# Performance work log

Hardware: AMD Instinct MI355X
Metric: run time of the kernel (lower is better)

## Reference

```python
import jax, jax.numpy as jnp
import numpy as np

EPS = 1e-12  # torch F.normalize eps


def setup_inputs() -> dict:
    key = jax.random.key(0)
    k1, k2, k3 = jax.random.split(key, 3)
    N, C, H, W = 64, 512, 30, 30
    K = 64
    x = jax.random.normal(k1, (N, C, H, W), dtype=jnp.float32)
    # 1x1 conv weight [K, C] (kernel spatial dims squeezed out)
    conv_w = jax.random.normal(k2, (K, C), dtype=jnp.float32) * 0.04
    centroids = jax.random.uniform(k3, (K, C), dtype=jnp.float32)
    return {"x": x, "conv_w": conv_w, "centroids": centroids}


def reference(x, conv_w, centroids):
    N, C, H, W = x.shape
    K = conv_w.shape[0]
    # descriptor-wise L2 normalize over channel dim (normalize_input=True)
    nrm = jnp.sqrt(jnp.sum(x * x, axis=1, keepdims=True))
    x = x / jnp.maximum(nrm, EPS)
    xf = x.reshape(N, C, H * W)                       # [N, C, P]
    # 1x1 conv == per-pixel matmul: [N, K, P]
    logits = jnp.einsum("kc,ncp->nkp", conv_w, xf)
    a = jax.nn.softmax(logits, axis=1)                # softmax over clusters
    # vlad[n,k,c] = sum_p a[n,k,p] * (xf[n,c,p] - centroids[k,c])
    #            = (a @ xf^T) - sum_p(a) * centroids   (GEMM decomposition)
    agg = jnp.einsum("nkp,ncp->nkc", a, xf)           # [N, K, C]
    vlad = agg - a.sum(axis=-1)[:, :, None] * centroids[None]
    return vlad
```

## Files before the change

kernel.cpp:

```cpp
#include <hip/hip_runtime.h>
#include <math.h>

#define N_DIM 64
#define C_DIM 512
#define K_DIM 64
#define P_DIM 900
#define P_PAD 928
#define PTILES 15

typedef __attribute__((ext_vector_type(8))) short short8;
typedef __attribute__((ext_vector_type(4))) float f32x4;
typedef __attribute__((ext_vector_type(4))) uint  u32x4;

#define A2_ELEMS   ((size_t)N_DIM * K_DIM * P_PAD)

__device__ inline ushort f2bf(float f) {
  uint u = __builtin_bit_cast(uint, f);
  u += 0x7FFFu + ((u >> 16) & 1u);
  return (ushort)(u >> 16);
}
__device__ inline uint pk2(float a, float b) {
  return (uint)f2bf(a) | ((uint)f2bf(b) << 16);
}

__global__ __launch_bounds__(256, 2) void netvlad_assign(
    const float* __restrict__ x, const float* __restrict__ w,
    ushort* __restrict__ a2, float* __restrict__ asum_part)
{
  const int n = blockIdx.y, bpt = blockIdx.x, p0 = bpt * 64;
  const int tid = threadIdx.x, wave = tid >> 6, lane = tid & 63;
  const int l15 = lane & 15, lhi = lane >> 4;

  __shared__ float wredm[4][4][16];
  __shared__ float wreds[4][4][16];

  short8 wfrag[16];
  const float* wrow = w + (size_t)(wave * 16 + l15) * C_DIM + lhi * 8;
#pragma unroll
  for (int ks = 0; ks < 16; ++ks) {
    f32x4 f0 = *(const f32x4*)(wrow + ks * 32);
    f32x4 f1 = *(const f32x4*)(wrow + ks * 32 + 4);
    u32x4 up;
    up[0] = pk2(f0[0], f0[1]); up[1] = pk2(f0[2], f0[3]);
    up[2] = pk2(f1[0], f1[1]); up[3] = pk2(f1[2], f1[3]);
    wfrag[ks] = __builtin_bit_cast(short8, up);
  }

  const float* xb = x + (size_t)n * C_DIM * P_DIM;
  int pb = p0 + 4 * l15;
  if (pb > P_DIM - 4) pb = P_DIM - 4;
  const float* xbase = xb + pb + (size_t)(lhi * 8) * P_DIM;

  f32x4 acc[4];
#pragma unroll
  for (int pt = 0; pt < 4; ++pt) acc[pt] = (f32x4){0.f, 0.f, 0.f, 0.f};
  float ssqp[4] = {0.f, 0.f, 0.f, 0.f};

#pragma unroll
  for (int ks = 0; ks < 16; ++ks) {
    const float* src = xbase + (size_t)(ks * 32) * P_DIM;
    f32x4 xv0 = *(const f32x4*)(src + 0 * P_DIM);
    f32x4 xv1 = *(const f32x4*)(src + 1 * P_DIM);
    f32x4 xv2 = *(const f32x4*)(src + 2 * P_DIM);
    f32x4 xv3 = *(const f32x4*)(src + 3 * P_DIM);
    f32x4 xv4 = *(const f32x4*)(src + 4 * P_DIM);
    f32x4 xv5 = *(const f32x4*)(src + 5 * P_DIM);
    f32x4 xv6 = *(const f32x4*)(src + 6 * P_DIM);
    f32x4 xv7 = *(const f32x4*)(src + 7 * P_DIM);
#pragma unroll
    for (int pt = 0; pt < 4; ++pt) {
      ssqp[pt] += xv0[pt] * xv0[pt] + xv1[pt] * xv1[pt]
                + xv2[pt] * xv2[pt] + xv3[pt] * xv3[pt]
                + xv4[pt] * xv4[pt] + xv5[pt] * xv5[pt]
                + xv6[pt] * xv6[pt] + xv7[pt] * xv7[pt];
      u32x4 up;
      up[0] = pk2(xv0[pt], xv1[pt]); up[1] = pk2(xv2[pt], xv3[pt]);
      up[2] = pk2(xv4[pt], xv5[pt]); up[3] = pk2(xv6[pt], xv7[pt]);
      short8 xf = __builtin_bit_cast(short8, up);
      acc[pt] = __builtin_amdgcn_mfma_f32_16x16x32_bf16(wfrag[ks], xf, acc[pt], 0, 0, 0);
    }
  }

  float linv[4];
#pragma unroll
  for (int pt = 0; pt < 4; ++pt) {
    float s = ssqp[pt];
    s += __shfl_xor(s, 16);
    s += __shfl_xor(s, 32);
    linv[pt] = 1.0f / fmaxf(sqrtf(s), 1e-12f);
  }

  float lg[4][4];
#pragma unroll
  for (int pt = 0; pt < 4; ++pt) {
    float m = -1e30f;
#pragma unroll
    for (int r = 0; r < 4; ++r) { lg[pt][r] = acc[pt][r] * linv[pt]; m = fmaxf(m, lg[pt][r]); }
    m = fmaxf(m, __shfl_xor(m, 16));
    m = fmaxf(m, __shfl_xor(m, 32));
    if (lhi == 0) wredm[wave][pt][l15] = m;
  }
  __syncthreads();
#pragma unroll
  for (int pt = 0; pt < 4; ++pt) {
    float m = fmaxf(fmaxf(wredm[0][pt][l15], wredm[1][pt][l15]),
                    fmaxf(wredm[2][pt][l15], wredm[3][pt][l15]));
    float s = 0.f;
#pragma unroll
    for (int r = 0; r < 4; ++r) { lg[pt][r] = __expf(lg[pt][r] - m); s += lg[pt][r]; }
    s += __shfl_xor(s, 16);
    s += __shfl_xor(s, 32);
    if (lhi == 0) wreds[wave][pt][l15] = s;
  }
  __syncthreads();

  ushort* a2b = a2 + (size_t)n * K_DIM * P_PAD;
  float asr[4] = {0.f, 0.f, 0.f, 0.f};
#pragma unroll
  for (int pt = 0; pt < 4; ++pt) {
    float stot = wreds[0][pt][l15] + wreds[1][pt][l15] +
                 wreds[2][pt][l15] + wreds[3][pt][l15];
    float rs = 1.0f / stot;
    int p = p0 + 4 * l15 + pt;
    bool vv = p < P_DIM;
#pragma unroll
    for (int r = 0; r < 4; ++r) {
      float a = lg[pt][r] * rs;
      if (vv) asr[r] += a;
      if (p < P_PAD) {
        int k = wave * 16 + lhi * 4 + r;
        a2b[(size_t)k * P_PAD + p] = vv ? f2bf(a * linv[pt]) : (ushort)0;
      }
    }
  }
#pragma unroll
  for (int r = 0; r < 4; ++r) {
    float v = asr[r];
    v += __shfl_xor(v, 1); v += __shfl_xor(v, 2);
    v += __shfl_xor(v, 4); v += __shfl_xor(v, 8);
    if (l15 == 0) {
      int k = wave * 16 + lhi * 4 + r;
      asum_part[((size_t)n * K_DIM + k) * PTILES + bpt] = v;
    }
  }
}

__global__ __launch_bounds__(256, 4) void netvlad_agg(
    const float* __restrict__ x, const ushort* __restrict__ a2,
    const float* __restrict__ asum_part, const float* __restrict__ cent,
    float* __restrict__ out)
{
  const int n = blockIdx.y, ct = blockIdx.x, c0 = ct * 64;
  const int tid = threadIdx.x, wave = tid >> 6, lane = tid & 63;
  const int l15 = lane & 15, lhi = lane >> 4;

  __shared__ float asum_s[64];
  if (tid < 64) {
    const float* ap = asum_part + ((size_t)n * K_DIM + tid) * PTILES;
    float s = 0.f;
#pragma unroll
    for (int j = 0; j < PTILES; ++j) s += ap[j];
    asum_s[tid] = s;
  }
  __syncthreads();

  f32x4 acc[4];
#pragma unroll
  for (int mt = 0; mt < 4; ++mt) acc[mt] = (f32x4){0.f, 0.f, 0.f, 0.f};

  const float*  xrow = x + (size_t)n * C_DIM * P_DIM
                         + (size_t)(c0 + wave * 16 + l15) * P_DIM;
  const ushort* ab   = a2 + (size_t)n * K_DIM * P_PAD;

  for (int ks = 0; ks < 29; ++ks) {
    int pb = ks * 32 + lhi * 8;
    short8 bfrag;
    if (pb + 8 <= P_DIM) {
      f32x4 f0 = *(const f32x4*)(xrow + pb);
      f32x4 f1 = *(const f32x4*)(xrow + pb + 4);
      u32x4 up;
      up[0] = pk2(f0[0], f0[1]); up[1] = pk2(f0[2], f0[3]);
      up[2] = pk2(f1[0], f1[1]); up[3] = pk2(f1[2], f1[3]);
      bfrag = __builtin_bit_cast(short8, up);
    } else {
#pragma unroll
      for (int j = 0; j < 8; ++j)
        bfrag[j] = (pb + j < P_DIM) ? (short)f2bf(xrow[pb + j]) : (short)0;
    }
#pragma unroll
    for (int mt = 0; mt < 4; ++mt) {
      short8 afrag = *(const short8*)(ab + (size_t)(mt * 16 + l15) * P_PAD
                                         + ks * 32 + lhi * 8);
      acc[mt] = __builtin_amdgcn_mfma_f32_16x16x32_bf16(afrag, bfrag, acc[mt], 0, 0, 0);
    }
  }

  const int c = c0 + wave * 16 + l15;
#pragma unroll
  for (int mt = 0; mt < 4; ++mt) {
#pragma unroll
    for (int r = 0; r < 4; ++r) {
      int k = mt * 16 + lhi * 4 + r;
      out[((size_t)n * K_DIM + k) * C_DIM + c] =
          acc[mt][r] - asum_s[k] * cent[(size_t)k * C_DIM + c];
    }
  }
}

extern "C" void kernel_launch(void* const* d_in, const int* in_sizes, int n_in,
                              void* d_out, int out_size, void* d_ws, size_t ws_size,
                              hipStream_t stream) {
  const float* x    = (const float*)d_in[0];
  const float* w    = (const float*)d_in[1];
  const float* cent = (const float*)d_in[2];
  float* out = (float*)d_out;

  ushort* a2        = (ushort*)d_ws;
  float*  asum_part = (float*)((char*)d_ws + A2_ELEMS * sizeof(ushort));

  netvlad_assign<<<dim3(PTILES, N_DIM), 256, 0, stream>>>(x, w, a2, asum_part);
  netvlad_agg   <<<dim3(8, N_DIM),      256, 0, stream>>>(x, a2, asum_part, cent, out);
}
```

Before: 83.90 us.

## Split channel reduction across two wave groups in assign kernel

The assign kernel now launches 512 threads per block, with two halves each covering 256 of the 512 channels. The second half writes its partial MFMA accumulators and sum-of-squares to shared memory, and the first half adds them before running the softmax and output stage. This halves the per-wave serial K-loop and weight-fragment registers, so more waves can be in flight to hide global-load latency. The cost is an extra shared-memory round trip and barrier, and half the waves sit idle during the epilogue.

New measurement: 89.95 us. 1.07x slower.

```diff
diff --git a/kernel.cpp b/kernel.cpp
--- a/kernel.cpp
+++ b/kernel.cpp
@@ -23,21 +23,24 @@
   return (uint)f2bf(a) | ((uint)f2bf(b) << 16);
 }
 
-__global__ __launch_bounds__(256, 2) void netvlad_assign(
+__global__ __launch_bounds__(512, 6) void netvlad_assign(
     const float* __restrict__ x, const float* __restrict__ w,
     ushort* __restrict__ a2, float* __restrict__ asum_part)
 {
   const int n = blockIdx.y, bpt = blockIdx.x, p0 = bpt * 64;
-  const int tid = threadIdx.x, wave = tid >> 6, lane = tid & 63;
+  const int tid = threadIdx.x, wv = tid >> 6, lane = tid & 63;
+  const int kwave = wv & 3, chalf = wv >> 2;
   const int l15 = lane & 15, lhi = lane >> 4;
 
+  __shared__ f32x4 accs[4][4][64];
+  __shared__ float ssqs[4][4][64];
   __shared__ float wredm[4][4][16];
   __shared__ float wreds[4][4][16];
 
-  short8 wfrag[16];
-  const float* wrow = w + (size_t)(wave * 16 + l15) * C_DIM + lhi * 8;
-#pragma unroll
-  for (int ks = 0; ks < 16; ++ks) {
+  short8 wfrag[8];
+  const float* wrow = w + (size_t)(kwave * 16 + l15) * C_DIM + chalf * 256 + lhi * 8;
+#pragma unroll
+  for (int ks = 0; ks < 8; ++ks) {
     f32x4 f0 = *(const f32x4*)(wrow + ks * 32);
     f32x4 f1 = *(const f32x4*)(wrow + ks * 32 + 4);
     u32x4 up;
@@ -49,7 +52,7 @@
   const float* xb = x + (size_t)n * C_DIM * P_DIM;
   int pb = p0 + 4 * l15;
   if (pb > P_DIM - 4) pb = P_DIM - 4;
-  const float* xbase = xb + pb + (size_t)(lhi * 8) * P_DIM;
+  const float* xbase = xb + pb + (size_t)(chalf * 256 + lhi * 8) * P_DIM;
 
   f32x4 acc[4];
 #pragma unroll
@@ -57,7 +60,7 @@
   float ssqp[4] = {0.f, 0.f, 0.f, 0.f};
 
 #pragma unroll
-  for (int ks = 0; ks < 16; ++ks) {
+  for (int ks = 0; ks < 8; ++ks) {
     const float* src = xbase + (size_t)(ks * 32) * P_DIM;
     f32x4 xv0 = *(const f32x4*)(src + 0 * P_DIM);
     f32x4 xv1 = *(const f32x4*)(src + 1 * P_DIM);
@@ -81,66 +84,85 @@
     }
   }
 
+  if (chalf) {
+#pragma unroll
+    for (int pt = 0; pt < 4; ++pt) {
+      accs[kwave][pt][lane] = acc[pt];
+      ssqs[kwave][pt][lane] = ssqp[pt];
+    }
+  }
+  __syncthreads();
+
   float linv[4];
-#pragma unroll
-  for (int pt = 0; pt < 4; ++pt) {
-    float s = ssqp[pt];
-    s += __shfl_xor(s, 16);
-    s += __shfl_xor(s, 32);
-    linv[pt] = 1.0f / fmaxf(sqrtf(s), 1e-12f);
-  }
-
   float lg[4][4];
-#pragma unroll
-  for (int pt = 0; pt < 4; ++pt) {
-    float m = -1e30f;
-#pragma unroll
-    for (int r = 0; r < 4; ++r) { lg[pt][r] = acc[pt][r] * linv[pt]; m = fmaxf(m, lg[pt][r]); }
-    m = fmaxf(m, __shfl_xor(m, 16));
-    m = fmaxf(m, __shfl_xor(m, 32));
-    if (lhi == 0) wredm[wave][pt][l15] = m;
-  }
-  __syncthreads();
-#pragma unroll
-  for (int pt = 0; pt < 4; ++pt) {
-    float m = fmaxf(fmaxf(wredm[0][pt][l15], wredm[1][pt][l15]),
-                    fmaxf(wredm[2][pt][l15], wredm[3][pt][l15]));
-    float s = 0.f;
-#pragma unroll
-    for (int r = 0; r < 4; ++r) { lg[pt][r] = __expf(lg[pt][r] - m); s += lg[pt][r]; }
-    s += __shfl_xor(s, 16);
-    s += __shfl_xor(s, 32);
-    if (lhi == 0) wreds[wave][pt][l15] = s;
-  }
-  __syncthreads();
-
-  ushort* a2b = a2 + (size_t)n * K_DIM * P_PAD;
-  float asr[4] = {0.f, 0.f, 0.f, 0.f};
-#pragma unroll
-  for (int pt = 0; pt < 4; ++pt) {
-    float stot = wreds[0][pt][l15] + wreds[1][pt][l15] +
-                 wreds[2][pt][l15] + wreds[3][pt][l15];
-    float rs = 1.0f / stot;
-    int p = p0 + 4 * l15 + pt;
-    bool vv = p < P_DIM;
+  if (!chalf) {
+#pragma unroll
+    for (int pt = 0; pt < 4; ++pt) {
+      acc[pt] += accs[kwave][pt][lane];
+      ssqp[pt] += ssqs[kwave][pt][lane];
+    }
+#pragma unroll
+    for (int pt = 0; pt < 4; ++pt) {
+      float s = ssqp[pt];
+      s += __shfl_xor(s, 16);
+      s += __shfl_xor(s, 32);
+      linv[pt] = 1.0f / fmaxf(sqrtf(s), 1e-12f);
+    }
+#pragma unroll
+    for (int pt = 0; pt < 4; ++pt) {
+      float m = -1e30f;
+#pragma unroll
+      for (int r = 0; r < 4; ++r) { lg[pt][r] = acc[pt][r] * linv[pt]; m = fmaxf(m, lg[pt][r]); }
+      m = fmaxf(m, __shfl_xor(m, 16));
+      m = fmaxf(m, __shfl_xor(m, 32));
+      if (lhi == 0) wredm[kwave][pt][l15] = m;
+    }
+  }
+  __syncthreads();
+  if (!chalf) {
+#pragma unroll
+    for (int pt = 0; pt < 4; ++pt) {
+      float m = fmaxf(fmaxf(wredm[0][pt][l15], wredm[1][pt][l15]),
+                      fmaxf(wredm[2][pt][l15], wredm[3][pt][l15]));
+      float s = 0.f;
+#pragma unroll
+      for (int r = 0; r < 4; ++r) { lg[pt][r] = __expf(lg[pt][r] - m); s += lg[pt][r]; }
+      s += __shfl_xor(s, 16);
+      s += __shfl_xor(s, 32);
+      if (lhi == 0) wreds[kwave][pt][l15] = s;
+    }
+  }
+  __syncthreads();
+
+  if (!chalf) {
+    ushort* a2b = a2 + (size_t)n * K_DIM * P_PAD;
+    float asr[4] = {0.f, 0.f, 0.f, 0.f};
+#pragma unroll
+    for (int pt = 0; pt < 4; ++pt) {
+      float stot = wreds[0][pt][l15] + wreds[1][pt][l15] +
+                   wreds[2][pt][l15] + wreds[3][pt][l15];
+      float rs = 1.0f / stot;
+      int p = p0 + 4 * l15 + pt;
+      bool vv = p < P_DIM;
+#pragma unroll
+      for (int r = 0; r < 4; ++r) {
+        float a = lg[pt][r] * rs;
+        if (vv) asr[r] += a;
+        if (p < P_PAD) {
+          int k = kwave * 16 + lhi * 4 + r;
+          a2b[(size_t)k * P_PAD + p] = vv ? f2bf(a * linv[pt]) : (ushort)0;
+        }
+      }
+    }
 #pragma unroll
     for (int r = 0; r < 4; ++r) {
-      float a = lg[pt][r] * rs;
-      if (vv) asr[r] += a;
-      if (p < P_PAD) {
-        int k = wave * 16 + lhi * 4 + r;
-        a2b[(size_t)k * P_PAD + p] = vv ? f2bf(a * linv[pt]) : (ushort)0;
+      float v = asr[r];
+      v += __shfl_xor(v, 1); v += __shfl_xor(v, 2);
+      v += __shfl_xor(v, 4); v += __shfl_xor(v, 8);
+      if (l15 == 0) {
+        int k = kwave * 16 + lhi * 4 + r;
+        asum_part[((size_t)n * K_DIM + k) * PTILES + bpt] = v;
       }
-    }
-  }
-#pragma unroll
-  for (int r = 0; r < 4; ++r) {
-    float v = asr[r];
-    v += __shfl_xor(v, 1); v += __shfl_xor(v, 2);
-    v += __shfl_xor(v, 4); v += __shfl_xor(v, 8);
-    if (l15 == 0) {
-      int k = wave * 16 + lhi * 4 + r;
-      asum_part[((size_t)n * K_DIM + k) * PTILES + bpt] = v;
     }
   }
 }
@@ -218,6 +240,6 @@
   ushort* a2        = (ushort*)d_ws;
   float*  asum_part = (float*)((char*)d_ws + A2_ELEMS * sizeof(ushort));
 
-  netvlad_assign<<<dim3(PTILES, N_DIM), 256, 0, stream>>>(x, w, a2, asum_part);
+  netvlad_assign<<<dim3(PTILES, N_DIM), 512, 0, stream>>>(x, w, a2, asum_part);
   netvlad_agg   <<<dim3(8, N_DIM),      256, 0, stream>>>(x, a2, asum_part, cent, out);
 }
```

## Pre-transpose x into bf16 MFMA fragment layout in a separate kernel

Applied to the files above, without the earlier changes.

Adds a transpose kernel that converts x to bf16 in the exact fragment order used by the assignment GEMM and writes per-channel-tile partial sums of squares. The assignment kernel then loads ready-made fragments and reduces the partial norms, instead of doing strided fp32 loads and converting in registers. This removes the strided access and the conversion work from the assignment kernel. The cost is an extra launch, a full extra read of x, and a write of a bf16 copy to workspace.

Result: slower. 91.35 us (+8.9%).

```diff
diff --git a/kernel.cpp b/kernel.cpp
--- a/kernel.cpp
+++ b/kernel.cpp
@@ -7,12 +7,16 @@
 #define P_DIM 900
 #define P_PAD 928
 #define PTILES 15
+#define CTILES 8
 
 typedef __attribute__((ext_vector_type(8))) short short8;
 typedef __attribute__((ext_vector_type(4))) float f32x4;
 typedef __attribute__((ext_vector_type(4))) uint  u32x4;
 
 #define A2_ELEMS   ((size_t)N_DIM * K_DIM * P_PAD)
+#define ASUM_ELEMS ((size_t)N_DIM * K_DIM * PTILES)
+#define SSQ_ELEMS  ((size_t)CTILES * N_DIM * P_DIM)
+#define XTF_ELEMS  ((size_t)N_DIM * PTILES * 16 * 4 * 64 * 8)
 
 __device__ inline ushort f2bf(float f) {
   uint u = __builtin_bit_cast(uint, f);
@@ -23,14 +27,77 @@
   return (uint)f2bf(a) | ((uint)f2bf(b) << 16);
 }
 
+__global__ __launch_bounds__(256) void transpose_x(
+    const float* __restrict__ x, ushort* __restrict__ xtf,
+    float* __restrict__ ssq_part)
+{
+  const int ct = blockIdx.x, pt = blockIdx.y, n = blockIdx.z;
+  const int p0 = pt * 64, c0 = ct * 64, tid = threadIdx.x;
+  __shared__ float lds[64][68];
+  __shared__ float red[4][64];
+
+  const float* xb = x + ((size_t)n * C_DIM + c0) * P_DIM;
+  const int cl = tid >> 4;
+  const int p4 = (tid & 15) * 4;
+#pragma unroll
+  for (int pass = 0; pass < 4; ++pass) {
+    const int c = cl + pass * 16;
+    const int gp = p0 + p4;
+    float4 v;
+    if (gp + 4 <= P_DIM) {
+      v = *(const float4*)(xb + (size_t)c * P_DIM + gp);
+    } else {
+      v.x = (gp + 0 < P_DIM) ? xb[(size_t)c * P_DIM + gp + 0] : 0.f;
+      v.y = (gp + 1 < P_DIM) ? xb[(size_t)c * P_DIM + gp + 1] : 0.f;
+      v.z = (gp + 2 < P_DIM) ? xb[(size_t)c * P_DIM + gp + 2] : 0.f;
+      v.w = (gp + 3 < P_DIM) ? xb[(size_t)c * P_DIM + gp + 3] : 0.f;
+    }
+    *(float4*)&lds[c][p4] = v;
+  }
+  __syncthreads();
+
+  const int pl = tid & 63, co = tid >> 6;
+  float ssq = 0.f;
+  uint pk[8];
+#pragma unroll
+  for (int q = 0; q < 8; ++q) {
+    float a = lds[co * 16 + q * 2 + 0][pl];
+    float b = lds[co * 16 + q * 2 + 1][pl];
+    ssq += a * a + b * b;
+    pk[q] = pk2(a, b);
+  }
+  red[co][pl] = ssq;
+
+  const size_t fbase = ((size_t)n * PTILES + pt) * 16;
+#pragma unroll
+  for (int o = 0; o < 2; ++o) {
+    const int cg = c0 + co * 16 + o * 8;
+    const int ks  = cg >> 5;
+    const int lhi = (cg >> 3) & 3;
+    u32x4 wv;
+    wv[0] = pk[o * 4 + 0]; wv[1] = pk[o * 4 + 1];
+    wv[2] = pk[o * 4 + 2]; wv[3] = pk[o * 4 + 3];
+    *(u32x4*)(xtf + (((fbase + ks) * 4 + lhi) * 64 + pl) * 8) = wv;
+  }
+  __syncthreads();
+  if (tid < 64) {
+    int p = p0 + tid;
+    if (p < P_DIM)
+      ssq_part[((size_t)ct * N_DIM + n) * P_DIM + p] =
+          red[0][tid] + red[1][tid] + red[2][tid] + red[3][tid];
+  }
+}
+
 __global__ __launch_bounds__(256, 2) void netvlad_assign(
-    const float* __restrict__ x, const float* __restrict__ w,
+    const float* __restrict__ w, const ushort* __restrict__ xtf,
+    const float* __restrict__ ssq_part,
     ushort* __restrict__ a2, float* __restrict__ asum_part)
 {
   const int n = blockIdx.y, bpt = blockIdx.x, p0 = bpt * 64;
   const int tid = threadIdx.x, wave = tid >> 6, lane = tid & 63;
   const int l15 = lane & 15, lhi = lane >> 4;
 
+  __shared__ float invn_s[64];
   __shared__ float wredm[4][4][16];
   __shared__ float wreds[4][4][16];
 
@@ -46,53 +113,37 @@
     wfrag[ks] = __builtin_bit_cast(short8, up);
   }
 
-  const float* xb = x + (size_t)n * C_DIM * P_DIM;
-  int pb = p0 + 4 * l15;
-  if (pb > P_DIM - 4) pb = P_DIM - 4;
-  const float* xbase = xb + pb + (size_t)(lhi * 8) * P_DIM;
-
+  if (tid < 64) {
+    int p = p0 + tid;
+    float s = 0.f;
+    if (p < P_DIM) {
+#pragma unroll
+      for (int ct = 0; ct < CTILES; ++ct)
+        s += ssq_part[((size_t)ct * N_DIM + n) * P_DIM + p];
+    }
+    invn_s[tid] = 1.0f / fmaxf(sqrtf(s), 1e-12f);
+  }
+
+  const ushort* xf_base = xtf + ((size_t)n * PTILES + bpt) * 16 * 4 * 64 * 8;
   f32x4 acc[4];
 #pragma unroll
   for (int pt = 0; pt < 4; ++pt) acc[pt] = (f32x4){0.f, 0.f, 0.f, 0.f};
-  float ssqp[4] = {0.f, 0.f, 0.f, 0.f};
 
 #pragma unroll
   for (int ks = 0; ks < 16; ++ks) {
-    const float* src = xbase + (size_t)(ks * 32) * P_DIM;
-    f32x4 xv0 = *(const f32x4*)(src + 0 * P_DIM);
-    f32x4 xv1 = *(const f32x4*)(src + 1 * P_DIM);
-    f32x4 xv2 = *(const f32x4*)(src + 2 * P_DIM);
-    f32x4 xv3 = *(const f32x4*)(src + 3 * P_DIM);
-    f32x4 xv4 = *(const f32x4*)(src + 4 * P_DIM);
-    f32x4 xv5 = *(const f32x4*)(src + 5 * P_DIM);
-    f32x4 xv6 = *(const f32x4*)(src + 6 * P_DIM);
-    f32x4 xv7 = *(const f32x4*)(src + 7 * P_DIM);
 #pragma unroll
     for (int pt = 0; pt < 4; ++pt) {
-      ssqp[pt] += xv0[pt] * xv0[pt] + xv1[pt] * xv1[pt]
-                + xv2[pt] * xv2[pt] + xv3[pt] * xv3[pt]
-                + xv4[pt] * xv4[pt] + xv5[pt] * xv5[pt]
-                + xv6[pt] * xv6[pt] + xv7[pt] * xv7[pt];
-      u32x4 up;
-      up[0] = pk2(xv0[pt], xv1[pt]); up[1] = pk2(xv2[pt], xv3[pt]);
-      up[2] = pk2(xv4[pt], xv5[pt]); up[3] = pk2(xv6[pt], xv7[pt]);
-      short8 xf = __builtin_bit_cast(short8, up);
+      short8 xf = *(const short8*)(xf_base
+                    + (((size_t)ks * 4 + lhi) * 64 + pt * 16 + l15) * 8);
       acc[pt] = __builtin_amdgcn_mfma_f32_16x16x32_bf16(wfrag[ks], xf, acc[pt], 0, 0, 0);
     }
   }
-
-  float linv[4];
+  __syncthreads();
+
+  float linv[4], lg[4][4];
 #pragma unroll
   for (int pt = 0; pt < 4; ++pt) {
-    float s = ssqp[pt];
-    s += __shfl_xor(s, 16);
-    s += __shfl_xor(s, 32);
-    linv[pt] = 1.0f / fmaxf(sqrtf(s), 1e-12f);
-  }
-
-  float lg[4][4];
-#pragma unroll
-  for (int pt = 0; pt < 4; ++pt) {
+    linv[pt] = invn_s[pt * 16 + l15];
     float m = -1e30f;
 #pragma unroll
     for (int r = 0; r < 4; ++r) { lg[pt][r] = acc[pt][r] * linv[pt]; m = fmaxf(m, lg[pt][r]); }
@@ -121,7 +172,7 @@
     float stot = wreds[0][pt][l15] + wreds[1][pt][l15] +
                  wreds[2][pt][l15] + wreds[3][pt][l15];
     float rs = 1.0f / stot;
-    int p = p0 + 4 * l15 + pt;
+    int p = p0 + pt * 16 + l15;
     bool vv = p < P_DIM;
 #pragma unroll
     for (int r = 0; r < 4; ++r) {
@@ -215,9 +266,13 @@
   const float* cent = (const float*)d_in[2];
   float* out = (float*)d_out;
 
-  ushort* a2        = (ushort*)d_ws;
-  float*  asum_part = (float*)((char*)d_ws + A2_ELEMS * sizeof(ushort));
-
-  netvlad_assign<<<dim3(PTILES, N_DIM), 256, 0, stream>>>(x, w, a2, asum_part);
-  netvlad_agg   <<<dim3(8, N_DIM),      256, 0, stream>>>(x, a2, asum_part, cent, out);
-}
+  char* wsb = (char*)d_ws;
+  ushort* a2        = (ushort*)wsb;
+  float*  asum_part = (float*)(wsb + A2_ELEMS * sizeof(ushort));
+  float*  ssq_part  = asum_part + ASUM_ELEMS;
+  ushort* xtf       = (ushort*)((char*)(ssq_part + SSQ_ELEMS));
+
+  transpose_x   <<<dim3(CTILES, PTILES, N_DIM), 256, 0, stream>>>(x, xtf, ssq_part);
+  netvlad_assign<<<dim3(PTILES, N_DIM),         256, 0, stream>>>(w, xtf, ssq_part, a2, asum_part);
+  netvlad_agg   <<<dim3(CTILES, N_DIM),         256, 0, stream>>>(x, a2, asum_part, cent, out);
+}
```

## Stage x tiles in LDS via double-buffered global_load_lds in assign kernel

Applied to the files above, without the earlier changes.

Previously all four waves in the assign kernel loaded the same 32-row x slice straight from global memory, so each element was fetched four times. Now each block cooperatively copies the slice once into a double-buffered LDS tile using direct global-to-LDS loads, prefetching the next channel step while computing the current one. Every wave then reads its MFMA operands and its sum-of-squares inputs from LDS. The cost is two block barriers per channel step and extra LDS traffic. Overlap may also be limited if the compiler's wait before the barrier also waits on the just-issued prefetch.

Result: no change. 83.91 us (+0.0%).

```diff
diff --git a/kernel.cpp b/kernel.cpp
--- a/kernel.cpp
+++ b/kernel.cpp
@@ -23,19 +23,26 @@
   return (uint)f2bf(a) | ((uint)f2bf(b) << 16);
 }
 
+__device__ __forceinline__ void gload16(const float* g, float* lds_base) {
+  __builtin_amdgcn_global_load_lds(
+      (const __attribute__((address_space(1))) void*)g,
+      (__attribute__((address_space(3))) void*)lds_base, 16, 0, 0);
+}
+
 __global__ __launch_bounds__(256, 2) void netvlad_assign(
     const float* __restrict__ x, const float* __restrict__ w,
     ushort* __restrict__ a2, float* __restrict__ asum_part)
 {
   const int n = blockIdx.y, bpt = blockIdx.x, p0 = bpt * 64;
-  const int tid = threadIdx.x, wave = tid >> 6, lane = tid & 63;
+  const int tid = threadIdx.x, wv = tid >> 6, lane = tid & 63;
   const int l15 = lane & 15, lhi = lane >> 4;
 
+  __shared__ float xs[2][2048];
   __shared__ float wredm[4][4][16];
   __shared__ float wreds[4][4][16];
 
   short8 wfrag[16];
-  const float* wrow = w + (size_t)(wave * 16 + l15) * C_DIM + lhi * 8;
+  const float* wrow = w + (size_t)(wv * 16 + l15) * C_DIM + lhi * 8;
 #pragma unroll
   for (int ks = 0; ks < 16; ++ks) {
     f32x4 f0 = *(const f32x4*)(wrow + ks * 32);
@@ -47,39 +54,50 @@
   }
 
   const float* xb = x + (size_t)n * C_DIM * P_DIM;
-  int pb = p0 + 4 * l15;
-  if (pb > P_DIM - 4) pb = P_DIM - 4;
-  const float* xbase = xb + pb + (size_t)(lhi * 8) * P_DIM;
+  int pld = p0 + (lane & 15) * 4;
+  if (pld > P_DIM - 4) pld = P_DIM - 4;
+  const int rquad = lane >> 4;
+
+#define STAGE(b, ks)                                                          \
+  {                                                                           \
+    _Pragma("unroll")                                                         \
+    for (int i = 0; i < 2; ++i) {                                             \
+      int seg = wv + 4 * i;                                                   \
+      int rr  = seg * 4 + rquad;                                              \
+      gload16(xb + (size_t)((ks) * 32 + rr) * P_DIM + pld, &xs[b][seg * 256]);\
+    }                                                                         \
+  }
 
   f32x4 acc[4];
 #pragma unroll
   for (int pt = 0; pt < 4; ++pt) acc[pt] = (f32x4){0.f, 0.f, 0.f, 0.f};
   float ssqp[4] = {0.f, 0.f, 0.f, 0.f};
 
+  STAGE(0, 0);
 #pragma unroll
   for (int ks = 0; ks < 16; ++ks) {
-    const float* src = xbase + (size_t)(ks * 32) * P_DIM;
-    f32x4 xv0 = *(const f32x4*)(src + 0 * P_DIM);
-    f32x4 xv1 = *(const f32x4*)(src + 1 * P_DIM);
-    f32x4 xv2 = *(const f32x4*)(src + 2 * P_DIM);
-    f32x4 xv3 = *(const f32x4*)(src + 3 * P_DIM);
-    f32x4 xv4 = *(const f32x4*)(src + 4 * P_DIM);
-    f32x4 xv5 = *(const f32x4*)(src + 5 * P_DIM);
-    f32x4 xv6 = *(const f32x4*)(src + 6 * P_DIM);
-    f32x4 xv7 = *(const f32x4*)(src + 7 * P_DIM);
+    if (ks + 1 < 16) STAGE((ks + 1) & 1, ks + 1);
+    __syncthreads();
+    const float* buf = xs[ks & 1];
+    f32x4 rd[8];
+#pragma unroll
+    for (int j = 0; j < 8; ++j)
+      rd[j] = *(const f32x4*)&buf[(8 * lhi + j) * 64 + l15 * 4];
 #pragma unroll
     for (int pt = 0; pt < 4; ++pt) {
-      ssqp[pt] += xv0[pt] * xv0[pt] + xv1[pt] * xv1[pt]
-                + xv2[pt] * xv2[pt] + xv3[pt] * xv3[pt]
-                + xv4[pt] * xv4[pt] + xv5[pt] * xv5[pt]
-                + xv6[pt] * xv6[pt] + xv7[pt] * xv7[pt];
+      ssqp[pt] += rd[0][pt] * rd[0][pt] + rd[1][pt] * rd[1][pt]
+                + rd[2][pt] * rd[2][pt] + rd[3][pt] * rd[3][pt]
+                + rd[4][pt] * rd[4][pt] + rd[5][pt] * rd[5][pt]
+                + rd[6][pt] * rd[6][pt] + rd[7][pt] * rd[7][pt];
       u32x4 up;
-      up[0] = pk2(xv0[pt], xv1[pt]); up[1] = pk2(xv2[pt], xv3[pt]);
-      up[2] = pk2(xv4[pt], xv5[pt]); up[3] = pk2(xv6[pt], xv7[pt]);
+      up[0] = pk2(rd[0][pt], rd[1][pt]); up[1] = pk2(rd[2][pt], rd[3][pt]);
+      up[2] = pk2(rd[4][pt], rd[5][pt]); up[3] = pk2(rd[6][pt], rd[7][pt]);
       short8 xf = __builtin_bit_cast(short8, up);
       acc[pt] = __builtin_amdgcn_mfma_f32_16x16x32_bf16(wfrag[ks], xf, acc[pt], 0, 0, 0);
     }
-  }
+    __syncthreads();
+  }
+#undef STAGE
 
   float linv[4];
 #pragma unroll
@@ -98,7 +116,7 @@
     for (int r = 0; r < 4; ++r) { lg[pt][r] = acc[pt][r] * linv[pt]; m = fmaxf(m, lg[pt][r]); }
     m = fmaxf(m, __shfl_xor(m, 16));
     m = fmaxf(m, __shfl_xor(m, 32));
-    if (lhi == 0) wredm[wave][pt][l15] = m;
+    if (lhi == 0) wredm[wv][pt][l15] = m;
   }
   __syncthreads();
 #pragma unroll
@@ -110,7 +128,7 @@
     for (int r = 0; r < 4; ++r) { lg[pt][r] = __expf(lg[pt][r] - m); s += lg[pt][r]; }
     s += __shfl_xor(s, 16);
     s += __shfl_xor(s, 32);
-    if (lhi == 0) wreds[wave][pt][l15] = s;
+    if (lhi == 0) wreds[wv][pt][l15] = s;
   }
   __syncthreads();
 
@@ -128,7 +146,7 @@
       float a = lg[pt][r] * rs;
       if (vv) asr[r] += a;
       if (p < P_PAD) {
-        int k = wave * 16 + lhi * 4 + r;
+        int k = wv * 16 + lhi * 4 + r;
         a2b[(size_t)k * P_PAD + p] = vv ? f2bf(a * linv[pt]) : (ushort)0;
       }
     }
@@ -139,7 +157,7 @@
     v += __shfl_xor(v, 1); v += __shfl_xor(v, 2);
     v += __shfl_xor(v, 4); v += __shfl_xor(v, 8);
     if (l15 == 0) {
-      int k = wave * 16 + lhi * 4 + r;
+      int k = wv * 16 + lhi * 4 + r;
       asum_part[((size_t)n * K_DIM + k) * PTILES + bpt] = v;
     }
   }
```
